# Performance work log

Measured on AMD Instinct MI355X. Metric: run time of the kernel, lower is better.

Reference implementation:

```python
import jax, jax.numpy as jnp
import numpy as np

N = 500      # nodes
F = 32       # input features
H = 128      # hidden_dim
HEADS = 2
B = 4        # batch
T = 16       # time steps
E = 8000     # edges (before self loops)
BN_EPS = 1e-5


def setup_inputs() -> dict:
    key = jax.random.key(0)
    ks = jax.random.split(key, 16)
    r = lambda i, shp, s=0.1: jax.random.normal(ks[i], shp, jnp.float32) * s
    return {
        "x": jax.random.normal(ks[0], (B, T, N, F), jnp.float32),
        "edge_index": jax.random.randint(ks[1], (2, E), 0, N),
        "W_proj": r(2, (F, H)), "b_proj": jnp.zeros((H,), jnp.float32),
        "gat1_Wl": r(3, (F, HEADS * H)), "gat1_Wr": r(4, (F, HEADS * H)),
        "gat1_att": r(5, (HEADS, H)), "gat1_b": jnp.zeros((HEADS * H,), jnp.float32),
        "bn1_g": jnp.ones((HEADS * H,), jnp.float32), "bn1_b": jnp.zeros((HEADS * H,), jnp.float32),
        "gat2_Wl": r(6, (HEADS * H, H)), "gat2_Wr": r(7, (HEADS * H, H)),
        "gat2_att": r(8, (1, H)), "gat2_b": jnp.zeros((H,), jnp.float32),
        "bn2_g": jnp.ones((H,), jnp.float32), "bn2_b": jnp.zeros((H,), jnp.float32),
        "Wih0": r(9, (4 * H, H)), "Whh0": r(10, (4 * H, H)),
        "bih0": jnp.zeros((4 * H,), jnp.float32), "bhh0": jnp.zeros((4 * H,), jnp.float32),
        "Wih1": r(11, (4 * H, H)), "Whh1": r(12, (4 * H, H)),
        "bih1": jnp.zeros((4 * H,), jnp.float32), "bhh1": jnp.zeros((4 * H,), jnp.float32),
        "fc_W1": r(13, (H, H // 2)), "fc_b1": jnp.zeros((H // 2,), jnp.float32),
        "fc_W2": r(14, (H // 2, 1)), "fc_b2": jnp.zeros((1,), jnp.float32),
    }


def gatv2(h, src, dst, Wl, Wr, att, bias, heads, out_dim, concat):
    # h: [G, N, Fin]; edges src -> dst (PyG convention), self loops included.
    G, n, _ = h.shape
    xl = (h @ Wl).reshape(G, n, heads, out_dim)
    xr = (h @ Wr).reshape(G, n, heads, out_dim)
    e = jax.nn.leaky_relu(xl[:, src] + xr[:, dst], 0.2)        # [G,E,heads,C]
    logits = jnp.einsum('gehc,hc->geh', e, att)                # [G,E,heads]
    m = jnp.full((G, n, heads), -jnp.inf, logits.dtype).at[:, dst].max(logits)
    ex = jnp.exp(logits - m[:, dst])
    s = jnp.zeros((G, n, heads), logits.dtype).at[:, dst].add(ex)
    alpha = ex / (s[:, dst] + 1e-16)
    msg = xl[:, src] * alpha[..., None]                        # [G,E,heads,C]
    out = jnp.zeros((G, n, heads, out_dim), h.dtype).at[:, dst].add(msg)
    out = out.reshape(G, n, heads * out_dim) if concat else out.mean(axis=2)
    return out + bias


def batchnorm(h, g, b):
    # BatchNorm1d in training mode: stats over the node axis, per graph call.
    mean = h.mean(axis=1, keepdims=True)
    var = jnp.var(h, axis=1, keepdims=True)
    return (h - mean) * jax.lax.rsqrt(var + BN_EPS) * g + b


def lstm_layer(xs, Wih, Whh, bih, bhh):
    # xs: [T, BN, H] -> ys: [T, BN, H]; torch gate order i,f,g,o.
    BNsz = xs.shape[1]
    h0 = jnp.zeros((BNsz, H), xs.dtype)
    def step(carry, xt):
        h, c = carry
        gates = xt @ Wih.T + h @ Whh.T + bih + bhh
        i, f, g, o = jnp.split(gates, 4, axis=-1)
        c = jax.nn.sigmoid(f) * c + jax.nn.sigmoid(i) * jnp.tanh(g)
        h = jax.nn.sigmoid(o) * jnp.tanh(c)
        return (h, c), h
    _, ys = jax.lax.scan(step, (h0, h0), xs)
    return ys


def reference(x, edge_index, W_proj, b_proj, gat1_Wl, gat1_Wr, gat1_att, gat1_b,
              bn1_g, bn1_b, gat2_Wl, gat2_Wr, gat2_att, gat2_b, bn2_g, bn2_b,
              Wih0, Whh0, bih0, bhh0, Wih1, Whh1, bih1, bhh1,
              fc_W1, fc_b1, fc_W2, fc_b2):
    b, t, n, f = x.shape
    G = b * t
    loops = jnp.arange(n, dtype=edge_index.dtype)  # GATv2Conv add_self_loops=True
    src = jnp.concatenate([edge_index[0], loops])
    dst = jnp.concatenate([edge_index[1], loops])
    xg = x.reshape(G, n, f)  # fuse all (b,t) graph calls into one batched pass
    h = gatv2(xg, src, dst, gat1_Wl, gat1_Wr, gat1_att, gat1_b, HEADS, H, True)
    h = jax.nn.elu(batchnorm(h, bn1_g, bn1_b))  # dropout = identity (eval)
    h = gatv2(h, src, dst, gat2_Wl, gat2_Wr, gat2_att, gat2_b, 1, H, False)
    h = jax.nn.elu(batchnorm(h, bn2_g, bn2_b))
    h = h + (xg @ W_proj + b_proj)               # residual input projection
    # faithful to torch: spatial.view(b*n, t, H) is a raw reshape of [b,t,n,H]
    flat = h.reshape(b * n, t, H)
    xs = jnp.swapaxes(flat, 0, 1)                # [t, b*n, H]
    ys = lstm_layer(xs, Wih0, Whh0, bih0, bhh0)
    ys = lstm_layer(ys, Wih1, Whh1, bih1, bhh1)  # inter-layer dropout = identity
    last = ys[-1]                                # [b*n, H]
    out = jax.nn.relu(last @ fc_W1 + fc_b1) @ fc_W2 + fc_b2
    return out.reshape(b, n, -1)
```

## Files before the change

kernel.cpp:

```cpp
#include <hip/hip_runtime.h>
#include <hip/hip_bf16.h>
#include <math.h>

#define G_   64
#define NN_  500
#define FIN_ 32
#define HD_  128
#define C1_  256
#define E0_  8000
#define EP_  8500
#define TT_  16
#define NR_  2000

typedef __attribute__((ext_vector_type(8))) short bf16x8;
typedef __attribute__((ext_vector_type(4))) float f32x4;

__device__ __forceinline__ float fsig(float x)  { return 1.f / (1.f + __expf(-x)); }
__device__ __forceinline__ float ftanh(float x) {
    float e = __expf(fminf(fmaxf(2.f * x, -30.f), 30.f));
    return (e - 1.f) / (e + 1.f);
}
__device__ __forceinline__ unsigned short f2bf(float f) {
    unsigned int u = __float_as_uint(f);
    return (unsigned short)((u + 0x7FFFu + ((u >> 16) & 1u)) >> 16);
}
__device__ __forceinline__ float bf2f(unsigned short h) {
    return __uint_as_float(((unsigned int)h) << 16);
}

__global__ __launch_bounds__(512) void k_degscan(const int* __restrict__ ei,
                                                 int* __restrict__ rowptr, int* __restrict__ cursor) {
    __shared__ int degs[512];
    __shared__ int scan[512];
    int t = threadIdx.x;
    degs[t] = 0;
    __syncthreads();
    for (int e = t; e < EP_; e += 512) {
        int dst = e < E0_ ? ei[E0_ + e] : e - E0_;
        atomicAdd(&degs[dst], 1);
    }
    __syncthreads();
    int v = degs[t];
    scan[t] = v;
    __syncthreads();
    for (int off = 1; off < 512; off <<= 1) {
        int add = (t >= off) ? scan[t - off] : 0;
        __syncthreads();
        scan[t] += add;
        __syncthreads();
    }
    int ex = scan[t] - v;
    if (t < NN_) { rowptr[t] = ex; cursor[t] = ex; }
    if (t == NN_) rowptr[NN_] = ex;
}
__global__ void k_fill(const int* __restrict__ ei, int* __restrict__ cursor, int* __restrict__ eids) {
    int e = blockIdx.x * blockDim.x + threadIdx.x;
    if (e >= EP_) return;
    int dst = e < E0_ ? ei[E0_ + e] : e - E0_;
    int pos = atomicAdd(&cursor[dst], 1);
    eids[pos] = e;
}

__global__ void k_wt(const float* __restrict__ Whh0, const float* __restrict__ Wih0,
                     const float* __restrict__ Whh1, const float* __restrict__ Wih1,
                     unsigned short* __restrict__ WB0, unsigned short* __restrict__ WB1) {
    int layer = blockIdx.y;
    int n = blockIdx.x * 256 + threadIdx.x;
    const float* Wh = layer ? Whh1 : Whh0;
    const float* Wi = layer ? Wih1 : Wih0;
    unsigned short* WB = layer ? WB1 : WB0;
    int j = n & 7, col = (n >> 3) & 511, kb8 = n >> 12;
    int k = kb8 * 8 + j;
    float w = (k < 128) ? Wh[(size_t)col * 128 + k] : Wi[(size_t)col * 128 + (k - 128)];
    WB[n] = f2bf(w);
}

__global__ void k_wtg(const float* __restrict__ Wl1, const float* __restrict__ Wr1,
                      const float* __restrict__ Wp,  const float* __restrict__ W2l,
                      const float* __restrict__ W2r, unsigned short* __restrict__ out) {
    int t = blockIdx.x * 256 + threadIdx.x;
    if (t >= 86016) return;
    const float* W; int N, base, local, KN;
    if (t < 8192)       { W = Wl1; N = 256; base = 0;      local = t;         KN = 8192;  }
    else if (t < 16384) { W = Wr1; N = 256; base = 16384;  local = t - 8192;  KN = 8192;  }
    else if (t < 20480) { W = Wp;  N = 128; base = 32768;  local = t - 16384; KN = 4096;  }
    else if (t < 53248) { W = W2l; N = 128; base = 40960;  local = t - 20480; KN = 32768; }
    else                { W = W2r; N = 128; base = 106496; local = t - 53248; KN = 32768; }
    int k = local / N, n = local - k * N;
    float wv = W[local];
    int idx = ((k >> 3) * N + n) * 8 + (k & 7);
    unsigned short h = f2bf(wv);
    out[base + idx] = h;
    out[base + KN + idx] = f2bf(wv - bf2f(h));
}

__global__ __launch_bounds__(256) void k_mm1(
    const float* __restrict__ x, const unsigned short* __restrict__ WP,
    const float* __restrict__ bp,
    float* __restrict__ xl1, float* __restrict__ xr1, float* __restrict__ proj)
{
    int tid = threadIdx.x, lane = tid & 63, w = tid >> 6;
    int row = lane & 15, kg = lane >> 4;
    int rb = blockIdx.x * 64 + w * 16;
    const float* ap = &x[(size_t)(rb + row) * 32 + kg * 8];
    float4 a0 = *(const float4*)ap, a1 = *(const float4*)(ap + 4);
    union { unsigned short u[8]; bf16x8 v; } ah, al;
    {
        float av[8] = {a0.x,a0.y,a0.z,a0.w,a1.x,a1.y,a1.z,a1.w};
        #pragma unroll
        for (int j = 0; j < 8; ++j) {
            unsigned short hb = f2bf(av[j]);
            ah.u[j] = hb;
            al.u[j] = f2bf(av[j] - bf2f(hb));
        }
    }
    const int crow = kg * 4;
    #pragma unroll 4
    for (int nt = 0; nt < 16; ++nt) {
        int n = nt * 16 + row;
        int idx = (kg * 256 + n) * 8;
        bf16x8 bh = *(const bf16x8*)(WP + idx);
        bf16x8 bl = *(const bf16x8*)(WP + 8192 + idx);
        f32x4 acc = {0.f,0.f,0.f,0.f};
        acc = __builtin_amdgcn_mfma_f32_16x16x32_bf16(ah.v, bh, acc, 0, 0, 0);
        acc = __builtin_amdgcn_mfma_f32_16x16x32_bf16(al.v, bh, acc, 0, 0, 0);
        acc = __builtin_amdgcn_mfma_f32_16x16x32_bf16(ah.v, bl, acc, 0, 0, 0);
        #pragma unroll
        for (int r = 0; r < 4; ++r)
            xl1[(size_t)(rb + crow + r) * 256 + n] = acc[r];
    }
    #pragma unroll 4
    for (int nt = 0; nt < 16; ++nt) {
        int n = nt * 16 + row;
        int idx = (kg * 256 + n) * 8;
        bf16x8 bh = *(const bf16x8*)(WP + 16384 + idx);
        bf16x8 bl = *(const bf16x8*)(WP + 24576 + idx);
        f32x4 acc = {0.f,0.f,0.f,0.f};
        acc = __builtin_amdgcn_mfma_f32_16x16x32_bf16(ah.v, bh, acc, 0, 0, 0);
        acc = __builtin_amdgcn_mfma_f32_16x16x32_bf16(al.v, bh, acc, 0, 0, 0);
        acc = __builtin_amdgcn_mfma_f32_16x16x32_bf16(ah.v, bl, acc, 0, 0, 0);
        #pragma unroll
        for (int r = 0; r < 4; ++r)
            xr1[(size_t)(rb + crow + r) * 256 + n] = acc[r];
    }
    #pragma unroll 4
    for (int nt = 0; nt < 8; ++nt) {
        int n = nt * 16 + row;
        int idx = (kg * 128 + n) * 8;
        bf16x8 bh = *(const bf16x8*)(WP + 32768 + idx);
        bf16x8 bl = *(const bf16x8*)(WP + 36864 + idx);
        f32x4 acc = {0.f,0.f,0.f,0.f};
        acc = __builtin_amdgcn_mfma_f32_16x16x32_bf16(ah.v, bh, acc, 0, 0, 0);
        acc = __builtin_amdgcn_mfma_f32_16x16x32_bf16(al.v, bh, acc, 0, 0, 0);
        acc = __builtin_amdgcn_mfma_f32_16x16x32_bf16(ah.v, bl, acc, 0, 0, 0);
        float bv = bp[n];
        #pragma unroll
        for (int r = 0; r < 4; ++r)
            proj[(size_t)(rb + crow + r) * 128 + n] = acc[r] + bv;
    }
}

__global__ __launch_bounds__(512) void k_mm2(
    const float* __restrict__ h1, const unsigned short* __restrict__ WP,
    const float* __restrict__ sc1, const float* __restrict__ sh1,
    float* __restrict__ xl2, float* __restrict__ xr2)
{
    int tid = threadIdx.x, lane = tid & 63, w = tid >> 6;
    int wr = w >> 2, wc = w & 3;
    int row = lane & 15, kg = lane >> 4;
    int rb = blockIdx.x * 32 + wr * 16;
    int grow = rb + row;
    int g = grow / NN_;
    const float* scp = sc1 + g * 256;
    const float* shp = sh1 + g * 256;
    const int cb = wc * 32 + row;
    f32x4 aL0 = {0.f,0.f,0.f,0.f}, aL1 = {0.f,0.f,0.f,0.f};
    f32x4 aR0 = {0.f,0.f,0.f,0.f}, aR1 = {0.f,0.f,0.f,0.f};
    #pragma unroll 2
    for (int kt = 0; kt < 8; ++kt) {
        int k0 = kt * 32 + kg * 8;
        const float* hp = &h1[(size_t)grow * 256 + k0];
        float4 h0 = *(const float4*)hp, h4 = *(const float4*)(hp + 4);
        float4 s0 = *(const float4*)&scp[k0], s4 = *(const float4*)&scp[k0 + 4];
        float4 t0 = *(const float4*)&shp[k0], t4 = *(const float4*)&shp[k0 + 4];
        union { unsigned short u[8]; bf16x8 v; } ah, al;
        {
            float hv[8] = {h0.x,h0.y,h0.z,h0.w,h4.x,h4.y,h4.z,h4.w};
            float sv[8] = {s0.x,s0.y,s0.z,s0.w,s4.x,s4.y,s4.z,s4.w};
            float tv[8] = {t0.x,t0.y,t0.z,t0.w,t4.x,t4.y,t4.z,t4.w};
            #pragma unroll
            for (int j = 0; j < 8; ++j) {
                float v = hv[j] * sv[j] + tv[j];
                v = v > 0.f ? v : expm1f(v);
                unsigned short hb = f2bf(v);
                ah.u[j] = hb;
                al.u[j] = f2bf(v - bf2f(hb));
            }
        }
        int idx = ((kt * 4 + kg) * 128 + cb) * 8;
        bf16x8 bhL0 = *(const bf16x8*)(WP + 40960 + idx);
        bf16x8 blL0 = *(const bf16x8*)(WP + 73728 + idx);
        bf16x8 bhL1 = *(const bf16x8*)(WP + 40960 + idx + 128);
        bf16x8 blL1 = *(const bf16x8*)(WP + 73728 + idx + 128);
        bf16x8 bhR0 = *(const bf16x8*)(WP + 106496 + idx);
        bf16x8 blR0 = *(const bf16x8*)(WP + 139264 + idx);
        bf16x8 bhR1 = *(const bf16x8*)(WP + 106496 + idx + 128);
        bf16x8 blR1 = *(const bf16x8*)(WP + 139264 + idx + 128);
        aL0 = __builtin_amdgcn_mfma_f32_16x16x32_bf16(ah.v, bhL0, aL0, 0, 0, 0);
        aL0 = __builtin_amdgcn_mfma_f32_16x16x32_bf16(al.v, bhL0, aL0, 0, 0, 0);
        aL0 = __builtin_amdgcn_mfma_f32_16x16x32_bf16(ah.v, blL0, aL0, 0, 0, 0);
        aL1 = __builtin_amdgcn_mfma_f32_16x16x32_bf16(ah.v, bhL1, aL1, 0, 0, 0);
        aL1 = __builtin_amdgcn_mfma_f32_16x16x32_bf16(al.v, bhL1, aL1, 0, 0, 0);
        aL1 = __builtin_amdgcn_mfma_f32_16x16x32_bf16(ah.v, blL1, aL1, 0, 0, 0);
        aR0 = __builtin_amdgcn_mfma_f32_16x16x32_bf16(ah.v, bhR0, aR0, 0, 0, 0);
        aR0 = __builtin_amdgcn_mfma_f32_16x16x32_bf16(al.v, bhR0, aR0, 0, 0, 0);
        aR0 = __builtin_amdgcn_mfma_f32_16x16x32_bf16(ah.v, blR0, aR0, 0, 0, 0);
        aR1 = __builtin_amdgcn_mfma_f32_16x16x32_bf16(ah.v, bhR1, aR1, 0, 0, 0);
        aR1 = __builtin_amdgcn_mfma_f32_16x16x32_bf16(al.v, bhR1, aR1, 0, 0, 0);
        aR1 = __builtin_amdgcn_mfma_f32_16x16x32_bf16(ah.v, blR1, aR1, 0, 0, 0);
    }
    const int crow = kg * 4;
    #pragma unroll
    for (int r = 0; r < 4; ++r) {
        size_t orow = (size_t)(rb + crow + r);
        xl2[orow * 128 + wc * 32 + row]      = aL0[r];
        xl2[orow * 128 + wc * 32 + 16 + row] = aL1[r];
        xr2[orow * 128 + wc * 32 + row]      = aR0[r];
        xr2[orow * 128 + wc * 32 + 16 + row] = aR1[r];
    }
}

template<int NH, int CD>
__global__ __launch_bounds__(256) void k_gat(
    const float* __restrict__ xl, const float* __restrict__ xr,
    const float* __restrict__ att, const int* __restrict__ ei,
    const int* __restrict__ rowptr, const int* __restrict__ eids,
    const float* __restrict__ bias, float* __restrict__ out)
{
    const int BD = NH * CD;
    const int NC = BD / 64;
    int bs = (blockIdx.x & 7) * 1000 + (blockIdx.x >> 3);
    int wid = bs * 4 + (threadIdx.x >> 6);
    int lane = threadIdx.x & 63;
    if (wid >= G_ * NN_) return;
    int g = wid / NN_, dst = wid % NN_;
    size_t gbase = (size_t)g * NN_;
    int ch0 = lane * NC;

    float xr_[NC], att_[NC], acc[NC];
    {
        const float* xrp = &xr[(gbase + dst) * BD + ch0];
        #pragma unroll
        for (int j = 0; j < NC; ++j) { xr_[j] = xrp[j]; att_[j] = att[ch0 + j]; acc[j] = 0.f; }
    }
    float m = -1e30f, ssum = 0.f;
    int rs = rowptr[dst], re = rowptr[dst + 1];
    int efull = rs + ((re - rs) & ~3);

#define LOADROW(IDX, DSTV) { \
        int eid_ = eids[IDX]; \
        int src_ = eid_ < E0_ ? ei[eid_] : eid_ - E0_; \
        const float* xp_ = &xl[(gbase + src_) * BD + ch0]; \
        if constexpr (NC == 4) { float4 t_ = *(const float4*)xp_; DSTV[0]=t_.x; DSTV[1]=t_.y; DSTV[2]=t_.z; DSTV[3]=t_.w; } \
        else { float2 t_ = *(const float2*)xp_; DSTV[0]=t_.x; DSTV[1]=t_.y; } \
    }

    int i = rs;
    if (i < efull) {
        float n0[NC], n1[NC], n2[NC], n3[NC];
        LOADROW(i + 0, n0); LOADROW(i + 1, n1); LOADROW(i + 2, n2); LOADROW(i + 3, n3);
        while (i < efull) {
            float r0[NC], r1[NC], r2[NC], r3[NC];
            #pragma unroll
            for (int j = 0; j < NC; ++j) { r0[j]=n0[j]; r1[j]=n1[j]; r2[j]=n2[j]; r3[j]=n3[j]; }
            i += 4;
            if (i < efull) {
                LOADROW(i + 0, n0); LOADROW(i + 1, n1); LOADROW(i + 2, n2); LOADROW(i + 3, n3);
            }
            float p0 = 0.f, p1 = 0.f, p2 = 0.f, p3 = 0.f;
            #pragma unroll
            for (int j = 0; j < NC; ++j) {
                float v0 = r0[j] + xr_[j]; v0 = v0 > 0.f ? v0 : 0.2f * v0; p0 = fmaf(v0, att_[j], p0);
                float v1 = r1[j] + xr_[j]; v1 = v1 > 0.f ? v1 : 0.2f * v1; p1 = fmaf(v1, att_[j], p1);
                float v2 = r2[j] + xr_[j]; v2 = v2 > 0.f ? v2 : 0.2f * v2; p2 = fmaf(v2, att_[j], p2);
                float v3 = r3[j] + xr_[j]; v3 = v3 > 0.f ? v3 : 0.2f * v3; p3 = fmaf(v3, att_[j], p3);
            }
            #pragma unroll
            for (int o = (NH == 2 ? 16 : 32); o; o >>= 1) {
                p0 += __shfl_xor(p0, o);
                p1 += __shfl_xor(p1, o);
                p2 += __shfl_xor(p2, o);
                p3 += __shfl_xor(p3, o);
            }
            float gm = fmaxf(fmaxf(p0, p1), fmaxf(p2, p3));
            float nm = fmaxf(m, gm);
            float fo = __expf(m - nm);
            float e0 = __expf(p0 - nm), e1 = __expf(p1 - nm);
            float e2 = __expf(p2 - nm), e3 = __expf(p3 - nm);
            #pragma unroll
            for (int j = 0; j < NC; ++j)
                acc[j] = acc[j] * fo + e0 * r0[j] + e1 * r1[j] + e2 * r2[j] + e3 * r3[j];
            ssum = ssum * fo + (e0 + e1 + e2 + e3);
            m = nm;
        }
    }
    for (; i < re; ++i) {
        float cu[NC];
        LOADROW(i, cu);
        float p = 0.f;
        #pragma unroll
        for (int j = 0; j < NC; ++j) {
            float v = cu[j] + xr_[j];
            v = v > 0.f ? v : 0.2f * v;
            p = fmaf(v, att_[j], p);
        }
        #pragma unroll
        for (int o = (NH == 2 ? 16 : 32); o; o >>= 1) p += __shfl_xor(p, o);
        float nm = fmaxf(m, p);
        float fo = __expf(m - nm), en = __expf(p - nm);
        #pragma unroll
        for (int j = 0; j < NC; ++j) acc[j] = acc[j] * fo + en * cu[j];
        ssum = ssum * fo + en;
        m = nm;
    }
#undef LOADROW
    float inv = 1.f / (ssum + 1e-16f);
    float* op = &out[(gbase + dst) * BD + ch0];
    #pragma unroll
    for (int j = 0; j < NC; ++j) op[j] = acc[j] * inv + bias[ch0 + j];
}

template<int C>
__global__ __launch_bounds__(C * 4) void k_bnstats(
    const float* __restrict__ h, const float* __restrict__ gamma, const float* __restrict__ beta,
    float* __restrict__ scale, float* __restrict__ shift)
{
    int g = blockIdx.x;
    int c = threadIdx.x % C, q = threadIdx.x / C;
    __shared__ float ps[4][C], pss[4][C];
    float s = 0.f, ss = 0.f;
    for (int n = q * 125; n < (q + 1) * 125; ++n) {
        float v = h[((size_t)g * NN_ + n) * C + c];
        s += v; ss += v * v;
    }
    ps[q][c] = s; pss[q][c] = ss;
    __syncthreads();
    if (q == 0) {
        #pragma unroll
        for (int qq = 1; qq < 4; ++qq) { s += ps[qq][c]; ss += pss[qq][c]; }
        float m = s * (1.f / NN_);
        float var = ss * (1.f / NN_) - m * m;
        float r = rsqrtf(var + 1e-5f);
        float sc = r * gamma[c];
        scale[g * C + c] = sc;
        shift[g * C + c] = beta[c] - m * sc;
    }
}

__global__ void k_bn_elu_add4(const float* __restrict__ h2, const float* __restrict__ scale2,
                              const float* __restrict__ shift2, const float* __restrict__ proj,
                              float* __restrict__ hres) {
    int i4 = blockIdx.x * blockDim.x + threadIdx.x;
    if (i4 >= G_ * NN_ * HD_ / 4) return;
    int base = i4 * 4;
    int c = base & 127;
    int g = base / (NN_ * HD_);
    float4 hv = *(const float4*)&h2[base];
    float4 sc = *(const float4*)&scale2[g * 128 + c];
    float4 sh = *(const float4*)&shift2[g * 128 + c];
    float4 pv = *(const float4*)&proj[base];
    float v0 = hv.x * sc.x + sh.x; v0 = (v0 > 0.f ? v0 : expm1f(v0)) + pv.x;
    float v1 = hv.y * sc.y + sh.y; v1 = (v1 > 0.f ? v1 : expm1f(v1)) + pv.y;
    float v2 = hv.z * sc.z + sh.z; v2 = (v2 > 0.f ? v2 : expm1f(v2)) + pv.z;
    float v3 = hv.w * sc.w + sh.w; v3 = (v3 > 0.f ? v3 : expm1f(v3)) + pv.w;
    *(float4*)&hres[base] = make_float4(v0, v1, v2, v3);
}

#define GROW 516

__device__ __forceinline__ void mfma_gates8(
    const bf16x8* __restrict__ Fh_hi, const bf16x8* __restrict__ Fh_lo,
    const bf16x8* __restrict__ Fx_hi, const bf16x8* __restrict__ Fx_lo,
    const unsigned short* __restrict__ WB, float* __restrict__ gl,
    const float* __restrict__ bb, int lane, int w8)
{
    f32x4 acc[4] = {{0.f,0.f,0.f,0.f},{0.f,0.f,0.f,0.f},{0.f,0.f,0.f,0.f},{0.f,0.f,0.f,0.f}};
    const int row = lane & 15, kg = lane >> 4;
    const int cb = w8 * 64 + row;
    #pragma unroll 4
    for (int kt = 0; kt < 8; ++kt) {
        const bf16x8* Hh = (kt < 4) ? Fh_hi : Fx_hi;
        const bf16x8* Hl = (kt < 4) ? Fh_lo : Fx_lo;
        int fu = ((kt & 3) * 4 + kg) * 16 + row;
        bf16x8 ah = Hh[fu];
        bf16x8 al = Hl[fu];
        const unsigned short* ph = WB + ((size_t)(kt * 4 + kg) * 512 + cb) * 8;
        #pragma unroll
        for (int nt = 0; nt < 4; ++nt) {
            bf16x8 bh = *(const bf16x8*)(ph + nt * 128);
            acc[nt] = __builtin_amdgcn_mfma_f32_16x16x32_bf16(ah, bh, acc[nt], 0, 0, 0);
            acc[nt] = __builtin_amdgcn_mfma_f32_16x16x32_bf16(al, bh, acc[nt], 0, 0, 0);
        }
    }
    const int crow = kg * 4;
    #pragma unroll
    for (int nt = 0; nt < 4; ++nt)
        #pragma unroll
        for (int r = 0; r < 4; ++r)
            gl[(crow + r) * GROW + w8 * 64 + nt * 16 + row] = acc[nt][r] + bb[nt];
}

__device__ __forceinline__ void cell_frag(
    const float* __restrict__ gl, float* __restrict__ cs,
    bf16x8* __restrict__ Hhi, bf16x8* __restrict__ Hlo, int t256)
{
    int r = t256 & 15, kb8 = t256 >> 4;
    const float* gr = gl + r * GROW + kb8 * 8;
    float* cp = cs + (r * 128 + kb8 * 8);
    union { unsigned short u[8]; bf16x8 v; } hh, hl;
    float cv[8];
    #pragma unroll
    for (int j = 0; j < 8; ++j) {
        float iv = fsig(gr[j]);
        float fv = fsig(gr[128 + j]);
        float gv = ftanh(gr[256 + j]);
        float ov = fsig(gr[384 + j]);
        float cn = fv * cp[j] + iv * gv;
        cv[j] = cn;
        float hv = ov * ftanh(cn);
        unsigned short hb = f2bf(hv);
        hh.u[j] = hb;
        hl.u[j] = f2bf(hv - bf2f(hb));
    }
    #pragma unroll
    for (int j = 0; j < 8; ++j) cp[j] = cv[j];
    Hhi[t256] = hh.v;
    Hlo[t256] = hl.v;
}

__device__ __forceinline__ void stage_x_frag(
    const float* __restrict__ src_row,
    bf16x8* __restrict__ Xhi, bf16x8* __restrict__ Xlo, int t256)
{
    int kb8 = t256 >> 4;
    const float* sp = src_row + kb8 * 8;
    union { unsigned short u[8]; bf16x8 v; } hh, hl;
    #pragma unroll
    for (int j = 0; j < 8; ++j) {
        float v = sp[j];
        unsigned short hb = f2bf(v);
        hh.u[j] = hb;
        hl.u[j] = f2bf(v - bf2f(hb));
    }
    Xhi[t256] = hh.v;
    Xlo[t256] = hl.v;
}

__global__ __launch_bounds__(1024, 2) void k_lstm_all(
    const float* __restrict__ hres,
    const unsigned short* __restrict__ WB0, const unsigned short* __restrict__ WB1,
    const float* __restrict__ bih0, const float* __restrict__ bhh0,
    const float* __restrict__ bih1, const float* __restrict__ bhh1,
    const float* __restrict__ fcW1, const float* __restrict__ fcb1,
    const float* __restrict__ fcW2, const float* __restrict__ fcb2,
    float* __restrict__ out)
{
    __shared__ bf16x8 h1h[256], h1l[256], h2h[256], h2l[256], xh[256], xlo[256];
    __shared__ float c1s[16 * 128], c2s[16 * 128];
    __shared__ float glA[16 * GROW], glB[16 * GROW];
    int tid = threadIdx.x, lane = tid & 63, w = tid >> 6;
    int grp = w >> 3, w8 = w & 7;
    int r0 = blockIdx.x * 16;

    if (tid < 256) {
        bf16x8 z = {0,0,0,0,0,0,0,0};
        h1h[tid] = z; h1l[tid] = z; h2h[tid] = z; h2l[tid] = z;
    }
    for (int i = tid; i < 16 * 128; i += 1024) { c1s[i] = 0.f; c2s[i] = 0.f; }

    float bbL[4];
    #pragma unroll
    for (int nt = 0; nt < 4; ++nt) {
        int c = w8 * 64 + nt * 16 + (lane & 15);
        bbL[nt] = grp ? (bih1[c] + bhh1[c]) : (bih0[c] + bhh0[c]);
    }
    if (tid >= 512 && tid < 768) {
        int t256 = tid - 512;
        int r = t256 & 15;
        stage_x_frag(&hres[(size_t)((r0 + r) * 16 + 0) * 128], xh, xlo, t256);
    }
    __syncthreads();
    for (int t = 0; t <= TT_; ++t) {
        if (grp == 0) {
            if (t < TT_) mfma_gates8(h1h, h1l, xh, xlo, WB0, glA, bbL, lane, w8);
        } else {
            if (t >= 1)  mfma_gates8(h2h, h2l, h1h, h1l, WB1, glB, bbL, lane, w8);
        }
        __syncthreads();
        if (tid < 256) {
            if (t < TT_) cell_frag(glA, c1s, h1h, h1l, tid);
        } else if (tid < 512) {
            if (t >= 1)  cell_frag(glB, c2s, h2h, h2l, tid - 256);
        } else if (tid < 768) {
            if (t + 1 < TT_) {
                int t256 = tid - 512;
                int r = t256 & 15;
                stage_x_frag(&hres[(size_t)((r0 + r) * 16 + t + 1) * 128], xh, xlo, t256);
            }
        }
        __syncthreads();
    }
    if (tid < 512) {
        const unsigned short* h2hu = (const unsigned short*)h2h;
        const unsigned short* h2lu = (const unsigned short*)h2l;
        int fr = tid >> 5, j = tid & 31;
        float s0 = fcb1[j], s1 = fcb1[j + 32];
        #pragma unroll 8
        for (int k = 0; k < 128; ++k) {
            int fi = ((k >> 3) * 16 + fr) * 8 + (k & 7);
            float hv = bf2f(h2hu[fi]) + bf2f(h2lu[fi]);
            s0 += hv * fcW1[k * 64 + j];
            s1 += hv * fcW1[k * 64 + j + 32];
        }
        float p = fmaxf(s0, 0.f) * fcW2[j] + fmaxf(s1, 0.f) * fcW2[j + 32];
        #pragma unroll
        for (int o = 16; o; o >>= 1) p += __shfl_xor(p, o);
        if (j == 0) out[r0 + fr] = p + fcb2[0];
    }
}

static const size_t OFF_XL1  = 0;
static const size_t OFF_XR1  = 8192000;
static const size_t OFF_H1   = 16384000;
static const size_t OFF_XL2  = 24576000;
static const size_t OFF_XR2  = 28672000;
static const size_t OFF_H2   = 32768000;
static const size_t OFF_PRJ  = 36864000;
static const size_t OFF_HRES = 40960000;
static const size_t OFF_SC1  = 45056000;
static const size_t OFF_SH1  = 45072384;
static const size_t OFF_SC2  = 45088768;
static const size_t OFF_SH2  = 45096960;
static const size_t OFF_WT0  = 45105152;
static const size_t OFF_WT1  = 45236224;
static const size_t OFF_WGP  = 45367296;
static const size_t OFF_INT  = 45453312;

extern "C" void kernel_launch(void* const* d_in, const int* in_sizes, int n_in,
                              void* d_out, int out_size, void* d_ws, size_t ws_size,
                              hipStream_t stream) {
    const float* x        = (const float*)d_in[0];
    const int*   ei       = (const int*)  d_in[1];
    const float* W_proj   = (const float*)d_in[2];
    const float* b_proj   = (const float*)d_in[3];
    const float* gat1_Wl  = (const float*)d_in[4];
    const float* gat1_Wr  = (const float*)d_in[5];
    const float* gat1_att = (const float*)d_in[6];
    const float* gat1_b   = (const float*)d_in[7];
    const float* bn1_g    = (const float*)d_in[8];
    const float* bn1_b    = (const float*)d_in[9];
    const float* gat2_Wl  = (const float*)d_in[10];
    const float* gat2_Wr  = (const float*)d_in[11];
    const float* gat2_att = (const float*)d_in[12];
    const float* gat2_b   = (const float*)d_in[13];
    const float* bn2_g    = (const float*)d_in[14];
    const float* bn2_b    = (const float*)d_in[15];
    const float* Wih0     = (const float*)d_in[16];
    const float* Whh0     = (const float*)d_in[17];
    const float* bih0     = (const float*)d_in[18];
    const float* bhh0     = (const float*)d_in[19];
    const float* Wih1     = (const float*)d_in[20];
    const float* Whh1     = (const float*)d_in[21];
    const float* bih1     = (const float*)d_in[22];
    const float* bhh1     = (const float*)d_in[23];
    const float* fc_W1    = (const float*)d_in[24];
    const float* fc_b1    = (const float*)d_in[25];
    const float* fc_W2    = (const float*)d_in[26];
    const float* fc_b2    = (const float*)d_in[27];
    float* out = (float*)d_out;

    float* ws = (float*)d_ws;
    float* xl1  = ws + OFF_XL1;
    float* xr1  = ws + OFF_XR1;
    float* h1   = ws + OFF_H1;
    float* xl2  = ws + OFF_XL2;
    float* xr2  = ws + OFF_XR2;
    float* h2   = ws + OFF_H2;
    float* proj = ws + OFF_PRJ;
    float* hres = ws + OFF_HRES;
    float* sc1  = ws + OFF_SC1;
    float* sh1  = ws + OFF_SH1;
    float* sc2  = ws + OFF_SC2;
    float* sh2  = ws + OFF_SH2;
    unsigned short* WB0 = (unsigned short*)(ws + OFF_WT0);
    unsigned short* WB1 = (unsigned short*)(ws + OFF_WT1);
    unsigned short* WGP = (unsigned short*)(ws + OFF_WGP);

    int* ibase  = (int*)(ws + OFF_INT);
    int* rowptr = ibase;
    int* cursor = ibase + 512;
    int* eids   = ibase + 1024;

    k_degscan<<<1, 512, 0, stream>>>(ei, rowptr, cursor);
    k_fill<<<(EP_ + 255) / 256, 256, 0, stream>>>(ei, cursor, eids);
    k_wt<<<dim3(512, 2), 256, 0, stream>>>(Whh0, Wih0, Whh1, Wih1, WB0, WB1);
    k_wtg<<<336, 256, 0, stream>>>(gat1_Wl, gat1_Wr, W_proj, gat2_Wl, gat2_Wr, WGP);

    k_mm1<<<500, 256, 0, stream>>>(x, WGP, b_proj, xl1, xr1, proj);
    k_gat<2, HD_><<<8000, 256, 0, stream>>>(xl1, xr1, gat1_att, ei, rowptr, eids, gat1_b, h1);
    k_bnstats<C1_><<<G_, C1_ * 4, 0, stream>>>(h1, bn1_g, bn1_b, sc1, sh1);

    k_mm2<<<1000, 512, 0, stream>>>(h1, WGP, sc1, sh1, xl2, xr2);
    k_gat<1, HD_><<<8000, 256, 0, stream>>>(xl2, xr2, gat2_att, ei, rowptr, eids, gat2_b, h2);
    k_bnstats<HD_><<<G_, HD_ * 4, 0, stream>>>(h2, bn2_g, bn2_b, sc2, sh2);

    k_bn_elu_add4<<<(G_ * NN_ * HD_ / 4 + 255) / 256, 256, 0, stream>>>(h2, sc2, sh2, proj, hres);

    k_lstm_all<<<125, 1024, 0, stream>>>(hres, WB0, WB1, bih0, bhh0, bih1, bhh1,
                                         fc_W1, fc_b1, fc_W2, fc_b2, out);
}
```

Baseline: 351.3 us.

## Fuse LSTM cell update into MFMA epilogue with register cell state and double buffering

Each wave now owns matching i/f/g/o gate columns, so the LSTM cell update runs directly on the MFMA accumulators. The cell state stays in registers instead of shared memory. This removes the shared gate buffers and one of the two barriers per timestep. Hidden and input fragments are double-buffered in shared memory to avoid read/write hazards within a step, at the cost of scattered 2-byte LDS stores.

```diff
diff --git a/kernel.cpp b/kernel.cpp
--- a/kernel.cpp
+++ b/kernel.cpp
@@ -376,86 +376,6 @@
     *(float4*)&hres[base] = make_float4(v0, v1, v2, v3);
 }
 
-#define GROW 516
-
-__device__ __forceinline__ void mfma_gates8(
-    const bf16x8* __restrict__ Fh_hi, const bf16x8* __restrict__ Fh_lo,
-    const bf16x8* __restrict__ Fx_hi, const bf16x8* __restrict__ Fx_lo,
-    const unsigned short* __restrict__ WB, float* __restrict__ gl,
-    const float* __restrict__ bb, int lane, int w8)
-{
-    f32x4 acc[4] = {{0.f,0.f,0.f,0.f},{0.f,0.f,0.f,0.f},{0.f,0.f,0.f,0.f},{0.f,0.f,0.f,0.f}};
-    const int row = lane & 15, kg = lane >> 4;
-    const int cb = w8 * 64 + row;
-    #pragma unroll 4
-    for (int kt = 0; kt < 8; ++kt) {
-        const bf16x8* Hh = (kt < 4) ? Fh_hi : Fx_hi;
-        const bf16x8* Hl = (kt < 4) ? Fh_lo : Fx_lo;
-        int fu = ((kt & 3) * 4 + kg) * 16 + row;
-        bf16x8 ah = Hh[fu];
-        bf16x8 al = Hl[fu];
-        const unsigned short* ph = WB + ((size_t)(kt * 4 + kg) * 512 + cb) * 8;
-        #pragma unroll
-        for (int nt = 0; nt < 4; ++nt) {
-            bf16x8 bh = *(const bf16x8*)(ph + nt * 128);
-            acc[nt] = __builtin_amdgcn_mfma_f32_16x16x32_bf16(ah, bh, acc[nt], 0, 0, 0);
-            acc[nt] = __builtin_amdgcn_mfma_f32_16x16x32_bf16(al, bh, acc[nt], 0, 0, 0);
-        }
-    }
-    const int crow = kg * 4;
-    #pragma unroll
-    for (int nt = 0; nt < 4; ++nt)
-        #pragma unroll
-        for (int r = 0; r < 4; ++r)
-            gl[(crow + r) * GROW + w8 * 64 + nt * 16 + row] = acc[nt][r] + bb[nt];
-}
-
-__device__ __forceinline__ void cell_frag(
-    const float* __restrict__ gl, float* __restrict__ cs,
-    bf16x8* __restrict__ Hhi, bf16x8* __restrict__ Hlo, int t256)
-{
-    int r = t256 & 15, kb8 = t256 >> 4;
-    const float* gr = gl + r * GROW + kb8 * 8;
-    float* cp = cs + (r * 128 + kb8 * 8);
-    union { unsigned short u[8]; bf16x8 v; } hh, hl;
-    float cv[8];
-    #pragma unroll
-    for (int j = 0; j < 8; ++j) {
-        float iv = fsig(gr[j]);
-        float fv = fsig(gr[128 + j]);
-        float gv = ftanh(gr[256 + j]);
-        float ov = fsig(gr[384 + j]);
-        float cn = fv * cp[j] + iv * gv;
-        cv[j] = cn;
-        float hv = ov * ftanh(cn);
-        unsigned short hb = f2bf(hv);
-        hh.u[j] = hb;
-        hl.u[j] = f2bf(hv - bf2f(hb));
-    }
-    #pragma unroll
-    for (int j = 0; j < 8; ++j) cp[j] = cv[j];
-    Hhi[t256] = hh.v;
-    Hlo[t256] = hl.v;
-}
-
-__device__ __forceinline__ void stage_x_frag(
-    const float* __restrict__ src_row,
-    bf16x8* __restrict__ Xhi, bf16x8* __restrict__ Xlo, int t256)
-{
-    int kb8 = t256 >> 4;
-    const float* sp = src_row + kb8 * 8;
-    union { unsigned short u[8]; bf16x8 v; } hh, hl;
-    #pragma unroll
-    for (int j = 0; j < 8; ++j) {
-        float v = sp[j];
-        unsigned short hb = f2bf(v);
-        hh.u[j] = hb;
-        hl.u[j] = f2bf(v - bf2f(hb));
-    }
-    Xhi[t256] = hh.v;
-    Xlo[t256] = hl.v;
-}
-
 __global__ __launch_bounds__(1024, 2) void k_lstm_all(
     const float* __restrict__ hres,
     const unsigned short* __restrict__ WB0, const unsigned short* __restrict__ WB1,
@@ -465,54 +385,112 @@
     const float* __restrict__ fcW2, const float* __restrict__ fcb2,
     float* __restrict__ out)
 {
-    __shared__ bf16x8 h1h[256], h1l[256], h2h[256], h2l[256], xh[256], xlo[256];
-    __shared__ float c1s[16 * 128], c2s[16 * 128];
-    __shared__ float glA[16 * GROW], glB[16 * GROW];
+    __shared__ bf16x8 h1h[2][256], h1l[2][256], h2h[2][256], h2l[2][256];
+    __shared__ bf16x8 xh[2][256], xlo[2][256];
     int tid = threadIdx.x, lane = tid & 63, w = tid >> 6;
     int grp = w >> 3, w8 = w & 7;
+    int row = lane & 15, kg = lane >> 4;
+    int col = w8 * 16 + row;
     int r0 = blockIdx.x * 16;
 
-    if (tid < 256) {
+    if (tid < 512) {
         bf16x8 z = {0,0,0,0,0,0,0,0};
-        h1h[tid] = z; h1l[tid] = z; h2h[tid] = z; h2l[tid] = z;
-    }
-    for (int i = tid; i < 16 * 128; i += 1024) { c1s[i] = 0.f; c2s[i] = 0.f; }
-
-    float bbL[4];
-    #pragma unroll
-    for (int nt = 0; nt < 4; ++nt) {
-        int c = w8 * 64 + nt * 16 + (lane & 15);
-        bbL[nt] = grp ? (bih1[c] + bhh1[c]) : (bih0[c] + bhh0[c]);
-    }
-    if (tid >= 512 && tid < 768) {
-        int t256 = tid - 512;
-        int r = t256 & 15;
-        stage_x_frag(&hres[(size_t)((r0 + r) * 16 + 0) * 128], xh, xlo, t256);
+        ((bf16x8*)h1h)[tid] = z; ((bf16x8*)h1l)[tid] = z;
+        ((bf16x8*)h2h)[tid] = z; ((bf16x8*)h2l)[tid] = z;
+    }
+
+    const float* bihp = grp ? bih1 : bih0;
+    const float* bhhp = grp ? bhh1 : bhh0;
+    float bb0 = bihp[col]       + bhhp[col];
+    float bb1 = bihp[128 + col] + bhhp[128 + col];
+    float bb2 = bihp[256 + col] + bhhp[256 + col];
+    float bb3 = bihp[384 + col] + bhhp[384 + col];
+    const unsigned short* WB = grp ? WB1 : WB0;
+
+    float cr0 = 0.f, cr1 = 0.f, cr2 = 0.f, cr3 = 0.f;
+
+    {
+        int lr = tid >> 6, hc2 = tid & 63;
+        float2 v = *(const float2*)&hres[((size_t)(r0 + lr) * 16 + 0) * 128 + hc2 * 2];
+        unsigned short* XH = (unsigned short*)xh[0];
+        unsigned short* XL = (unsigned short*)xlo[0];
+        int hc = hc2 * 2, fu = (hc >> 3) * 16 + lr, j = hc & 7;
+        unsigned short hb = f2bf(v.x);
+        XH[fu * 8 + j] = hb; XL[fu * 8 + j] = f2bf(v.x - bf2f(hb));
+        hc = hc2 * 2 + 1; fu = (hc >> 3) * 16 + lr; j = hc & 7;
+        hb = f2bf(v.y);
+        XH[fu * 8 + j] = hb; XL[fu * 8 + j] = f2bf(v.y - bf2f(hb));
     }
     __syncthreads();
+
     for (int t = 0; t <= TT_; ++t) {
-        if (grp == 0) {
-            if (t < TT_) mfma_gates8(h1h, h1l, xh, xlo, WB0, glA, bbL, lane, w8);
-        } else {
-            if (t >= 1)  mfma_gates8(h2h, h2l, h1h, h1l, WB1, glB, bbL, lane, w8);
+        int pr = t & 1, pw = pr ^ 1;
+        bool active = grp ? (t >= 1) : (t < TT_);
+        if (active) {
+            const bf16x8* Ahh = grp ? h2h[pr] : h1h[pr];
+            const bf16x8* Ahl = grp ? h2l[pr] : h1l[pr];
+            const bf16x8* Axh = grp ? h1h[pr] : xh[pr];
+            const bf16x8* Axl = grp ? h1l[pr] : xlo[pr];
+            f32x4 a0 = {0.f,0.f,0.f,0.f}, a1 = {0.f,0.f,0.f,0.f};
+            f32x4 a2 = {0.f,0.f,0.f,0.f}, a3 = {0.f,0.f,0.f,0.f};
+            #pragma unroll 4
+            for (int kt = 0; kt < 8; ++kt) {
+                const bf16x8* Hh = (kt < 4) ? Ahh : Axh;
+                const bf16x8* Hl = (kt < 4) ? Ahl : Axl;
+                int fu = ((kt & 3) * 4 + kg) * 16 + row;
+                bf16x8 ah = Hh[fu];
+                bf16x8 al = Hl[fu];
+                const unsigned short* ph = WB + ((size_t)(kt * 4 + kg) * 512 + col) * 8;
+                bf16x8 b0 = *(const bf16x8*)(ph);
+                bf16x8 b1 = *(const bf16x8*)(ph + 1024);
+                bf16x8 b2 = *(const bf16x8*)(ph + 2048);
+                bf16x8 b3 = *(const bf16x8*)(ph + 3072);
+                a0 = __builtin_amdgcn_mfma_f32_16x16x32_bf16(ah, b0, a0, 0, 0, 0);
+                a0 = __builtin_amdgcn_mfma_f32_16x16x32_bf16(al, b0, a0, 0, 0, 0);
+                a1 = __builtin_amdgcn_mfma_f32_16x16x32_bf16(ah, b1, a1, 0, 0, 0);
+                a1 = __builtin_amdgcn_mfma_f32_16x16x32_bf16(al, b1, a1, 0, 0, 0);
+                a2 = __builtin_amdgcn_mfma_f32_16x16x32_bf16(ah, b2, a2, 0, 0, 0);
+                a2 = __builtin_amdgcn_mfma_f32_16x16x32_bf16(al, b2, a2, 0, 0, 0);
+                a3 = __builtin_amdgcn_mfma_f32_16x16x32_bf16(ah, b3, a3, 0, 0, 0);
+                a3 = __builtin_amdgcn_mfma_f32_16x16x32_bf16(al, b3, a3, 0, 0, 0);
+            }
+            unsigned short* HU = (unsigned short*)(grp ? h2h[pw] : h1h[pw]);
+            unsigned short* LU = (unsigned short*)(grp ? h2l[pw] : h1l[pw]);
+            const int fub = (col >> 3) * 16;
+            const int jj = col & 7;
+            #pragma unroll
+            for (int r = 0; r < 4; ++r) {
+                float gi = a0[r] + bb0;
+                float gf = a1[r] + bb1;
+                float gg = a2[r] + bb2;
+                float go = a3[r] + bb3;
+                float cold = (r == 0) ? cr0 : (r == 1) ? cr1 : (r == 2) ? cr2 : cr3;
+                float cn = fsig(gf) * cold + fsig(gi) * ftanh(gg);
+                if (r == 0) cr0 = cn; else if (r == 1) cr1 = cn; else if (r == 2) cr2 = cn; else cr3 = cn;
+                float hv = fsig(go) * ftanh(cn);
+                int lrow = kg * 4 + r;
+                unsigned short hb = f2bf(hv);
+                HU[(fub + lrow) * 8 + jj] = hb;
+                LU[(fub + lrow) * 8 + jj] = f2bf(hv - bf2f(hb));
+            }
+        }
+        if (t + 1 < TT_) {
+            int lr = tid >> 6, hc2 = tid & 63;
+            float2 v = *(const float2*)&hres[((size_t)(r0 + lr) * 16 + (t + 1)) * 128 + hc2 * 2];
+            unsigned short* XH = (unsigned short*)xh[pw];
+            unsigned short* XL = (unsigned short*)xlo[pw];
+            int hc = hc2 * 2, fu = (hc >> 3) * 16 + lr, j = hc & 7;
+            unsigned short hb = f2bf(v.x);
+            XH[fu * 8 + j] = hb; XL[fu * 8 + j] = f2bf(v.x - bf2f(hb));
+            hc = hc2 * 2 + 1; fu = (hc >> 3) * 16 + lr; j = hc & 7;
+            hb = f2bf(v.y);
+            XH[fu * 8 + j] = hb; XL[fu * 8 + j] = f2bf(v.y - bf2f(hb));
         }
         __syncthreads();
-        if (tid < 256) {
-            if (t < TT_) cell_frag(glA, c1s, h1h, h1l, tid);
-        } else if (tid < 512) {
-            if (t >= 1)  cell_frag(glB, c2s, h2h, h2l, tid - 256);
-        } else if (tid < 768) {
-            if (t + 1 < TT_) {
-                int t256 = tid - 512;
-                int r = t256 & 15;
-                stage_x_frag(&hres[(size_t)((r0 + r) * 16 + t + 1) * 128], xh, xlo, t256);
-            }
-        }
-        __syncthreads();
     }
     if (tid < 512) {
-        const unsigned short* h2hu = (const unsigned short*)h2h;
-        const unsigned short* h2lu = (const unsigned short*)h2l;
+        const unsigned short* h2hu = (const unsigned short*)h2h[1];
+        const unsigned short* h2lu = (const unsigned short*)h2l[1];
         int fr = tid >> 5, j = tid & 31;
         float s0 = fcb1[j], s1 = fcb1[j + 32];
         #pragma unroll 8
```

New measurement: 336.4 us (median of 2 runs). 1.04x faster.
